# Optimization experiments

Hardware: AMD Instinct MI355X
Metric: run time of the kernel (lower is better)

Reference implementation:

```python
import jax, jax.numpy as jnp
import numpy as np

B, N, E = 4096, 32, 64
IN_DIM, H = 74, 256
ADD_DIM = 2
MLP1, MLP2 = 1024, 512
GCR_LAYERS = 5


def setup_inputs() -> dict:
    key = jax.random.key(0)
    ks = jax.random.split(key, 26)
    s = 0.05
    inp = {
        "x": jax.random.normal(ks[0], (B, N, IN_DIM), jnp.float32),
        "add_features": jax.random.normal(ks[1], (B, ADD_DIM), jnp.float32),
        "src": jax.random.randint(ks[2], (B, E), 0, N, jnp.int32),
        "dst": jax.random.randint(ks[3], (B, E), 0, N, jnp.int32),
        # first GraphConv (in_dim -> hidden)
        "W_in": jax.random.normal(ks[4], (IN_DIM, H), jnp.float32) * s,
        "b_in": jnp.zeros((H,), jnp.float32),
        # 5 GCR blocks, each with two GraphConv layers (hidden -> hidden)
        "W_g1": jax.random.normal(ks[5], (GCR_LAYERS, H, H), jnp.float32) * s,
        "b_g1": jnp.zeros((GCR_LAYERS, H), jnp.float32),
        "W_g2": jax.random.normal(ks[6], (GCR_LAYERS, H, H), jnp.float32) * s,
        "b_g2": jnp.zeros((GCR_LAYERS, H), jnp.float32),
        # attention pooling
        "Wq": jax.random.normal(ks[7], (H, H), jnp.float32) * s,
        "bq": jnp.zeros((H,), jnp.float32),
        "Wk": jax.random.normal(ks[8], (H, H), jnp.float32) * s,
        "bk": jnp.zeros((H,), jnp.float32),
        "Wv": jax.random.normal(ks[9], (H, 1), jnp.float32) * s,
        "bv": jnp.zeros((1,), jnp.float32),
        "W_m1": jax.random.normal(ks[10], (H + ADD_DIM, MLP1), jnp.float32) * s,
        "b_m1": jnp.zeros((MLP1,), jnp.float32),
        "W_m2": jax.random.normal(ks[11], (MLP1, MLP2), jnp.float32) * s,
        "b_m2": jnp.zeros((MLP2,), jnp.float32),
        "W_m3": jax.random.normal(ks[12], (MLP2, 1), jnp.float32) * s,
        "b_m3": jnp.zeros((1,), jnp.float32),
    }
    return inp


def _forward(x, add_features, src, dst, W_in, b_in, W_g1, b_g1, W_g2, b_g2,
             Wq, bq, Wk, bk, Wv, bv, W_m1, b_m1, W_m2, b_m2, W_m3, b_m3):
    def per_graph(xg, sg, dg):
        # DGL GraphConv norm='both': D_out^{-1/2} on src side, D_in^{-1/2} on dst side
        ones = jnp.ones((E,), xg.dtype)
        out_deg = jnp.zeros((N,), xg.dtype).at[sg].add(ones)
        in_deg = jnp.zeros((N,), xg.dtype).at[dg].add(ones)
        onorm = jax.lax.rsqrt(jnp.clip(out_deg, 1.0))
        inorm = jax.lax.rsqrt(jnp.clip(in_deg, 1.0))

        def conv(h, W, b):
            h = (h * onorm[:, None]) @ W                      # [N, out]
            agg = jnp.zeros((N, W.shape[1]), h.dtype).at[dg].add(h[sg])
            return agg * inorm[:, None] + b

        h = conv(xg, W_in, b_in)
        for i in range(GCR_LAYERS):
            t = conv(h, W_g1[i], b_g1[i])
            t = conv(jax.nn.relu(t), W_g2[i], b_g2[i])
            h = jax.nn.relu(t)                                # GCR output (res_connection=0)
        # attention-weighted pooling over nodes
        q = h @ Wq + bq                                       # [N, H]
        k = h @ Wk + bk                                       # [N, H]
        v = h @ Wv + bv                                       # [N, 1]
        attn = jax.nn.softmax(q @ k.T, axis=1)                # [N, N]
        w = (attn @ v)[:, 0]                                  # [N]
        return h.T @ w                                        # [H]

    feats = jax.vmap(per_graph)(x, src, dst)                  # [B, H]
    z = jnp.concatenate([feats, add_features], axis=1)        # [B, H+ADD_DIM]
    z = jax.nn.leaky_relu(z @ W_m1 + b_m1)
    z = jax.nn.leaky_relu(z @ W_m2 + b_m2)
    z = z @ W_m3 + b_m3                                       # [B, 1]
    return z[:, 0]


def reference(x, add_features, src, dst, W_in, b_in, W_g1, b_g1, W_g2, b_g2,
              Wq, bq, Wk, bk, Wv, bv, W_m1, b_m1, W_m2, b_m2, W_m3, b_m3):
    return _forward(x, add_features, src, dst, W_in, b_in, W_g1, b_g1, W_g2, b_g2,
                    Wq, bq, Wk, bk, Wv, bv, W_m1, b_m1, W_m2, b_m2, W_m3, b_m3)
```

## Files before the change

kernel.cpp:

```cpp
#include <hip/hip_runtime.h>
#include <math.h>

#define BB     4096
#define NN     32
#define EE     64
#define INDIM  74
#define HH     256
#define GCR    5
#define M1     1024
#define M2     512
#define FDIM   258
#define ADDD   2
#define FSTR   288

typedef __attribute__((ext_vector_type(8))) _Float16 half8_t;
typedef __attribute__((ext_vector_type(4))) float float4_t;

#define MF16(a, b, c) __builtin_amdgcn_mfma_f32_16x16x32_f16((a), (b), (c), 0, 0, 0)
#define LO_SCALE 1024.0f
#define LO_INV   (1.0f / 1024.0f)

#define WS_FH     0
#define WS_WQK    4227072
#define WS_TVEC   4489216
#define WS_PK     4490240
#define PK_WIN_HI 0
#define PK_WIN_LO 24576
#define PK_G_BASE 49152
#define PK_G_STRIDE 131072
#define PK_WQK_HI 1359872
#define PK_WQK_LO (1359872 + 65536)
#define PK_W1P    1490944
#define PK_W2P    1785856

union H4 { unsigned long long u; _Float16 h[4]; };

__global__ void prep1_kernel(const float* __restrict__ Wq, const float* __restrict__ Wk,
                             const float* __restrict__ bq,
                             float* __restrict__ wqkf, float* __restrict__ tvec) {
  const int i = blockIdx.x, j = threadIdx.x;
  if (i < 256) {
    __shared__ float qrow[256];
    qrow[j] = Wq[i * 256 + j];
    __syncthreads();
    float s = 0.f;
    for (int c = 0; c < 256; ++c) s = fmaf(qrow[c], Wk[j * 256 + c], s);
    wqkf[i * 256 + j] = s;
  } else {
    float s = 0.f;
    for (int c = 0; c < 256; ++c) s = fmaf(Wk[j * 256 + c], bq[c], s);
    tvec[j] = s;
  }
}

template<int KS, int KREAL>
__device__ __forceinline__ void pack_one(const float* __restrict__ S,
                                         _Float16* __restrict__ hi,
                                         _Float16* __restrict__ lo, int local) {
  const int l = local & 63;
  const int nk = local >> 6;
  const int ks = nk % KS;
  const int nt = nk / KS;
  const int j = nt * 16 + (l & 15);
  const int kbase = ks * 32 + (l >> 4) * 8;
  half8_t h8, l8;
  #pragma unroll
  for (int i = 0; i < 8; ++i) {
    const int k = kbase + i;
    const float v = (k < KREAL) ? S[k * 256 + j] : 0.f;
    const _Float16 hb = (_Float16)v;
    h8[i] = hb;
    l8[i] = (_Float16)((v - (float)hb) * LO_SCALE);
  }
  *(half8_t*)(hi + (size_t)local * 8) = h8;
  *(half8_t*)(lo + (size_t)local * 8) = l8;
}

__global__ void prep2_kernel(const float* __restrict__ W_in,
                             const float* __restrict__ W_g1, const float* __restrict__ W_g2,
                             const float* __restrict__ wqkf, _Float16* __restrict__ pk) {
  const int cid = blockIdx.x * 256 + threadIdx.x;
  if (cid < 3072) {
    pack_one<3, 74>(W_in, pk + PK_WIN_HI, pk + PK_WIN_LO, cid);
  } else {
    const int m = (cid - 3072) >> 13;
    const int local = (cid - 3072) & 8191;
    _Float16* hi; const float* S;
    if (m < 10) {
      hi = pk + PK_G_BASE + (size_t)m * PK_G_STRIDE;
      S = (m < 5) ? (W_g1 + (size_t)m * 65536) : (W_g2 + (size_t)(m - 5) * 65536);
    } else {
      hi = pk + PK_WQK_HI;
      S = wqkf;
    }
    pack_one<8, 256>(S, hi, hi + 65536, local);
  }
}

template<int KS, int KREAL, int NCOL>
__device__ __forceinline__ void pack_flat(const float* __restrict__ S,
                                          _Float16* __restrict__ dst, int local) {
  const int l = local & 63;
  const int nk = local >> 6;
  const int ks = nk % KS;
  const int nt = nk / KS;
  const int j = nt * 16 + (l & 15);
  const int kbase = ks * 32 + (l >> 4) * 8;
  half8_t h8;
  #pragma unroll
  for (int i = 0; i < 8; ++i) {
    const int k = kbase + i;
    h8[i] = (_Float16)((k < KREAL) ? S[(size_t)k * NCOL + j] : 0.f);
  }
  *(half8_t*)(dst + (size_t)local * 8) = h8;
}

__global__ void prep3_kernel(const float* __restrict__ W1, const float* __restrict__ W2,
                             _Float16* __restrict__ pk) {
  const int cid = blockIdx.x * 256 + threadIdx.x;
  if (cid < 36864) {
    pack_flat<9, 258, 1024>(W1, pk + PK_W1P, cid);
  } else {
    pack_flat<32, 1024, 512>(W2, pk + PK_W2P, cid - 36864);
  }
}

template<int KS, bool RELU>
__device__ __forceinline__ void conv2x(
    _Float16* Hs, _Float16* Tb, const _Float16* NmF,
    const _Float16* __restrict__ Whi,
    const float* __restrict__ bias,
    int lane, int wv)
{
  const int g4 = lane >> 4, l15 = lane & 15;
  const int sw = l15 << 3;

  #pragma unroll
  for (int p = 0; p < 2; ++p) {
    const int nt = p * 8 + wv;
    float4_t th[2][2];
    #pragma unroll
    for (int a = 0; a < 2; ++a)
      #pragma unroll
      for (int b = 0; b < 2; ++b)
        th[a][b] = (float4_t){0.f, 0.f, 0.f, 0.f};
    #pragma unroll
    for (int ks = 0; ks < KS; ++ks) {
      const int off = ((nt * KS + ks) * 64 + lane) * 8;
      const half8_t wh = *(const half8_t*)(Whi + off);
      const int j0 = ks * 32 + g4 * 8;
      #pragma unroll
      for (int gi = 0; gi < 2; ++gi)
        #pragma unroll
        for (int mt = 0; mt < 2; ++mt) {
          const half8_t ha = *(const half8_t*)(Hs + (gi << 13) + ((mt * 16 + l15) * 256 + (j0 ^ sw)));
          th[gi][mt] = MF16(ha, wh, th[gi][mt]);
        }
    }
    #pragma unroll
    for (int gi = 0; gi < 2; ++gi)
      #pragma unroll
      for (int mt = 0; mt < 2; ++mt) {
        const int r0 = mt * 16 + 4 * g4;
        H4 pk4;
        #pragma unroll
        for (int jj = 0; jj < 4; ++jj)
          pk4.h[jj] = (_Float16)th[gi][mt][jj];
        const int idx = nt * 512 + ((r0 >> 3) * 16 + l15) * 8 + (r0 & 7);
        *(unsigned long long*)(Tb + (gi << 13) + idx) = pk4.u;
      }
  }

  __syncthreads();

  #pragma unroll
  for (int p = 0; p < 2; ++p) {
    const int nt = p * 8 + wv;
    const float4 b4 = *(const float4*)&bias[nt * 16 + 4 * g4];
    const int j0 = nt * 16 + 4 * g4;
    #pragma unroll
    for (int gi = 0; gi < 2; ++gi) {
      const half8_t ta = *(const half8_t*)(Tb + (gi << 13) + nt * 512 + lane * 8);
      #pragma unroll
      for (int nt2 = 0; nt2 < 2; ++nt2) {
        const half8_t nmh = *(const half8_t*)(NmF + ((gi * 2 + nt2) * 64 + lane) * 8);
        const float4_t dh = MF16(ta, nmh, ((float4_t){0.f, 0.f, 0.f, 0.f}));
        H4 pk4;
        #pragma unroll
        for (int jj = 0; jj < 4; ++jj) {
          float v = dh[jj] + ((const float*)&b4)[jj];
          if (RELU) v = fmaxf(v, 0.f);
          pk4.h[jj] = (_Float16)v;
        }
        const int n = nt2 * 16 + l15;
        *(unsigned long long*)(Hs + (gi << 13) + (n * 256 + (j0 ^ ((n & 15) << 3)))) = pk4.u;
      }
    }
  }
  __syncthreads();
}

__global__ __launch_bounds__(512, 4)
void gnn_kernel(const float* __restrict__ x, const float* __restrict__ addf,
                const int* __restrict__ src, const int* __restrict__ dst,
                const float* __restrict__ b_in,
                const float* __restrict__ b_g1, const float* __restrict__ b_g2,
                const float* __restrict__ Wvp, const float* __restrict__ bv,
                const _Float16* __restrict__ pk,
                const float* __restrict__ tvec,
                _Float16* __restrict__ Fh)
{
  __shared__ __align__(16) _Float16 Hs[2][8192];
  __shared__ __align__(16) _Float16 Tb[2][8192];
  __shared__ __align__(16) _Float16 NmF[2048];
  __shared__ float Sb[2][1184];

  const int tid = threadIdx.x;
  const int lane = tid & 63;
  const int wv = tid >> 6;
  const int g4 = lane >> 4, l15 = lane & 15;
  const int sw = l15 << 3;
  const int ga = blockIdx.x * 2;

  for (int i = tid; i < 2048; i += 512) Sb[i >> 10][i & 1023] = 0.f;
  __syncthreads();
  if (tid < 128) {
    const int gi = tid >> 6, e = tid & 63;
    const int es = src[(size_t)(ga + gi) * EE + e];
    const int ed = dst[(size_t)(ga + gi) * EE + e];
    atomicAdd(&Sb[gi][ed * 32 + es], 1.0f);
  }
  __syncthreads();
  if (tid < 64) {
    const int gi = tid >> 5, n = tid & 31;
    float s = 0.f;
    for (int m = 0; m < NN; ++m) s += Sb[gi][n * 32 + m];
    Sb[gi][1056 + n] = 1.f / sqrtf(fmaxf(s, 1.f));
  } else if (tid < 128) {
    const int gi = (tid - 64) >> 5, n = tid & 31;
    float s = 0.f;
    for (int m = 0; m < NN; ++m) s += Sb[gi][m * 32 + n];
    Sb[gi][1088 + n] = 1.f / sqrtf(fmaxf(s, 1.f));
  }
  __syncthreads();
  for (int i = tid; i < 2048; i += 512) {
    const int gi = i >> 10, idx = i & 1023;
    Sb[gi][idx] *= Sb[gi][1056 + (idx >> 5)] * Sb[gi][1088 + (idx & 31)];
  }
  __syncthreads();

  if (wv == 0) {
    #pragma unroll
    for (int gi = 0; gi < 2; ++gi) {
      #pragma unroll
      for (int nt2 = 0; nt2 < 2; ++nt2) {
        half8_t h8;
        #pragma unroll
        for (int i = 0; i < 8; ++i)
          h8[i] = (_Float16)Sb[gi][(nt2 * 16 + l15) * 32 + g4 * 8 + i];
        *(half8_t*)(NmF + ((gi * 2 + nt2) * 64 + lane) * 8) = h8;
      }
    }
  }

  for (int i = tid; i < 2 * NN * 96; i += 512) {
    const int gi = i / 3072, rem = i - gi * 3072;
    const int r = rem / 96, c = rem - r * 96;
    const float vx = (c < INDIM) ? x[(size_t)(ga + gi) * (NN * INDIM) + r * INDIM + c] : 0.f;
    Hs[gi][r * 256 + (c ^ ((r & 15) << 3))] = (_Float16)vx;
  }
  __syncthreads();

  conv2x<3, false>(&Hs[0][0], &Tb[0][0], NmF, pk + PK_WIN_HI, b_in, lane, wv);
  #pragma unroll 1
  for (int L = 0; L < GCR; ++L) {
    conv2x<8, true>(&Hs[0][0], &Tb[0][0], NmF,
                    pk + PK_G_BASE + (size_t)L * PK_G_STRIDE, b_g1 + L * HH, lane, wv);
    conv2x<8, true>(&Hs[0][0], &Tb[0][0], NmF,
                    pk + PK_G_BASE + (size_t)(5 + L) * PK_G_STRIDE, b_g2 + L * HH, lane, wv);
  }

  {
    const _Float16* Qhi = pk + PK_WQK_HI;
    const int sgi = wv >> 2, smt = (wv >> 1) & 1, snt = wv & 1;
    float4_t sacc = (float4_t){0.f, 0.f, 0.f, 0.f};

    #pragma unroll
    for (int p = 0; p < 2; ++p) {
      const int nt = p * 8 + wv;
      float4_t uh[2][2];
      #pragma unroll
      for (int a = 0; a < 2; ++a)
        #pragma unroll
        for (int b = 0; b < 2; ++b)
          uh[a][b] = (float4_t){0.f, 0.f, 0.f, 0.f};
      #pragma unroll
      for (int ks = 0; ks < 8; ++ks) {
        const int off = ((nt * 8 + ks) * 64 + lane) * 8;
        const half8_t qh = *(const half8_t*)(Qhi + off);
        const int j0 = ks * 32 + g4 * 8;
        #pragma unroll
        for (int gi = 0; gi < 2; ++gi)
          #pragma unroll
          for (int mt = 0; mt < 2; ++mt) {
            const half8_t ha = *(const half8_t*)(&Hs[gi][(mt * 16 + l15) * 256 + (j0 ^ sw)]);
            uh[gi][mt] = MF16(ha, qh, uh[gi][mt]);
          }
      }
      const float tv = tvec[nt * 16 + l15];
      const int cl = wv * 16 + l15;
      #pragma unroll
      for (int gi = 0; gi < 2; ++gi)
        #pragma unroll
        for (int mt = 0; mt < 2; ++mt)
          #pragma unroll
          for (int jj = 0; jj < 4; ++jj) {
            const int n = mt * 16 + 4 * g4 + jj;
            Tb[gi][n * 128 + (cl ^ ((n & 15) << 3))] =
                (_Float16)(uh[gi][mt][jj] + tv);
          }
      __syncthreads();
      #pragma unroll
      for (int ksl = 0; ksl < 4; ++ksl) {
        const int kl = ksl * 32 + g4 * 8;
        const half8_t ua = *(const half8_t*)(&Tb[sgi][(smt * 16 + l15) * 128 + (kl ^ sw)]);
        const half8_t hb = *(const half8_t*)(&Hs[sgi][(snt * 16 + l15) * 256 + ((p * 128 + kl) ^ sw)]);
        sacc = MF16(ua, hb, sacc);
      }
      __syncthreads();
    }
    #pragma unroll
    for (int jj = 0; jj < 4; ++jj)
      Sb[sgi][(smt * 16 + 4 * g4 + jj) * 33 + snt * 16 + l15] = sacc[jj];
  }

  {
    const int gi = tid >> 8, m = (tid >> 3) & 31, q = tid & 7;
    float s = 0.f;
    const int c0 = q * 32;
    for (int cc = 0; cc < 32; ++cc) {
      const int c = c0 + cc;
      s = fmaf((float)Hs[gi][m * 256 + (c ^ ((m & 15) << 3))], Wvp[c], s);
    }
    s += __shfl_xor(s, 1);
    s += __shfl_xor(s, 2);
    s += __shfl_xor(s, 4);
    if (q == 0) Sb[gi][1120 + m] = s + bv[0];
  }
  __syncthreads();

  if (tid < 64) {
    const int gi = tid >> 5, n = tid & 31;
    float mx = -1e30f;
    #pragma unroll 1
    for (int m = 0; m < NN; ++m) mx = fmaxf(mx, Sb[gi][n * 33 + m]);
    float se = 0.f, sv = 0.f;
    #pragma unroll 1
    for (int m = 0; m < NN; ++m) {
      const float e = expf(Sb[gi][n * 33 + m] - mx);
      se += e;
      sv = fmaf(e, Sb[gi][1120 + m], sv);
    }
    Sb[gi][1152 + n] = sv / se;
  }
  __syncthreads();

  {
    const int gi = tid >> 8, j = tid & 255;
    float f0 = 0.f;
    #pragma unroll
    for (int m = 0; m < NN; ++m) {
      const float w = Sb[gi][1152 + m];
      f0 = fmaf((float)Hs[gi][m * 256 + (j ^ ((m & 15) << 3))], w, f0);
    }
    Fh[(size_t)(ga + gi) * FSTR + j] = (_Float16)f0;
    if (tid < 64) {
      const int g2 = tid >> 5, c = 256 + (tid & 31);
      Fh[(size_t)(ga + g2) * FSTR + c] =
          (c < FDIM) ? (_Float16)addf[(size_t)(ga + g2) * ADDD + (c - 256)] : (_Float16)0.f;
    }
  }
}

__global__ __launch_bounds__(512, 4)
void mlp_kernel(const _Float16* __restrict__ Fh,
                const _Float16* __restrict__ W1p, const float* __restrict__ b1,
                const _Float16* __restrict__ W2p, const float* __restrict__ b2,
                const float* __restrict__ W3, const float* __restrict__ b3,
                float* __restrict__ out)
{
  __shared__ __align__(16) _Float16 Ft[16 * 320];
  __shared__ __align__(16) _Float16 Z1[16 * 1024];
  __shared__ __align__(16) _Float16 Z2[16 * 512];

  const int tid = threadIdx.x, lane = tid & 63, wv = tid >> 6;
  const int g4 = lane >> 4, l15 = lane & 15;
  const int sw = (l15 & 7) << 3;
  const int r0 = blockIdx.x * 16;

  for (int i = tid; i < 16 * FSTR; i += 512) {
    const int r = i / FSTR, c = i - r * FSTR;
    Ft[r * 320 + (c ^ ((r & 7) << 3))] = Fh[(size_t)(r0 + r) * FSTR + c];
  }
  __syncthreads();

  {
    float4_t a1[8];
    #pragma unroll
    for (int t = 0; t < 8; ++t) a1[t] = (float4_t){0.f, 0.f, 0.f, 0.f};
    #pragma unroll
    for (int ks = 0; ks < 9; ++ks) {
      const half8_t fb = *(const half8_t*)(Ft + l15 * 320 + ((ks * 32 + g4 * 8) ^ sw));
      #pragma unroll
      for (int t = 0; t < 8; ++t) {
        const int jt = wv * 8 + t;
        const half8_t wf = *(const half8_t*)(W1p + ((size_t)(jt * 9 + ks) * 64 + lane) * 8);
        a1[t] = MF16(wf, fb, a1[t]);
      }
    }
    #pragma unroll
    for (int t = 0; t < 8; ++t) {
      const int j0 = (wv * 8 + t) * 16 + 4 * g4;
      const float4 bb = *(const float4*)&b1[j0];
      H4 pk4;
      #pragma unroll
      for (int jj = 0; jj < 4; ++jj) {
        const float z = a1[t][jj] + ((const float*)&bb)[jj];
        pk4.h[jj] = (_Float16)fmaxf(z, 0.01f * z);
      }
      *(unsigned long long*)(Z1 + l15 * 1024 + (j0 ^ sw)) = pk4.u;
    }
  }
  __syncthreads();

  {
    float4_t a2[4];
    #pragma unroll
    for (int t = 0; t < 4; ++t) a2[t] = (float4_t){0.f, 0.f, 0.f, 0.f};
    #pragma unroll 4
    for (int ks = 0; ks < 32; ++ks) {
      const half8_t zb = *(const half8_t*)(Z1 + l15 * 1024 + ((ks * 32 + g4 * 8) ^ sw));
      #pragma unroll
      for (int t = 0; t < 4; ++t) {
        const int jt = wv * 4 + t;
        const half8_t wf = *(const half8_t*)(W2p + ((size_t)(jt * 32 + ks) * 64 + lane) * 8);
        a2[t] = MF16(wf, zb, a2[t]);
      }
    }
    #pragma unroll
    for (int t = 0; t < 4; ++t) {
      const int j0 = (wv * 4 + t) * 16 + 4 * g4;
      const float4 bb = *(const float4*)&b2[j0];
      H4 pk4;
      #pragma unroll
      for (int jj = 0; jj < 4; ++jj) {
        const float z = a2[t][jj] + ((const float*)&bb)[jj];
        pk4.h[jj] = (_Float16)fmaxf(z, 0.01f * z);
      }
      *(unsigned long long*)(Z2 + l15 * 512 + (j0 ^ sw)) = pk4.u;
    }
  }
  __syncthreads();

  {
    const int m = tid >> 5, q = tid & 31;
    const int swm = (m & 7) << 3;
    float s = 0.f;
    #pragma unroll
    for (int h = 0; h < 2; ++h) {
      const int c0 = q * 16 + h * 8;
      const half8_t z8 = *(const half8_t*)(Z2 + m * 512 + (c0 ^ swm));
      #pragma unroll
      for (int i2 = 0; i2 < 8; ++i2)
        s = fmaf((float)z8[i2], W3[c0 + i2], s);
    }
    s += __shfl_xor(s, 1);
    s += __shfl_xor(s, 2);
    s += __shfl_xor(s, 4);
    s += __shfl_xor(s, 8);
    s += __shfl_xor(s, 16);
    if (q == 0) out[r0 + m] = s + b3[0];
  }
}

extern "C" void kernel_launch(void* const* d_in, const int* in_sizes, int n_in,
                              void* d_out, int out_size, void* d_ws, size_t ws_size,
                              hipStream_t stream) {
  (void)in_sizes; (void)n_in; (void)out_size; (void)ws_size;
  const float* x    = (const float*)d_in[0];
  const float* addf = (const float*)d_in[1];
  const int*   src  = (const int*)d_in[2];
  const int*   dst  = (const int*)d_in[3];
  const float* W_in = (const float*)d_in[4];
  const float* b_in = (const float*)d_in[5];
  const float* W_g1 = (const float*)d_in[6];
  const float* b_g1 = (const float*)d_in[7];
  const float* W_g2 = (const float*)d_in[8];
  const float* b_g2 = (const float*)d_in[9];
  const float* Wq   = (const float*)d_in[10];
  const float* bq   = (const float*)d_in[11];
  const float* Wk   = (const float*)d_in[12];
  const float* Wv   = (const float*)d_in[14];
  const float* bv   = (const float*)d_in[15];
  const float* W1   = (const float*)d_in[16];
  const float* b1   = (const float*)d_in[17];
  const float* W2   = (const float*)d_in[18];
  const float* b2   = (const float*)d_in[19];
  const float* W3   = (const float*)d_in[20];
  const float* b3   = (const float*)d_in[21];
  float* out = (float*)d_out;

  _Float16* Fh    = (_Float16*)((char*)d_ws + WS_FH);
  float* wqkf     = (float*)((char*)d_ws + WS_WQK);
  float* tvec     = (float*)((char*)d_ws + WS_TVEC);
  _Float16* pk    = (_Float16*)((char*)d_ws + WS_PK);

  prep1_kernel<<<dim3(257), dim3(256), 0, stream>>>(Wq, Wk, bq, wqkf, tvec);
  prep2_kernel<<<dim3(364), dim3(256), 0, stream>>>(W_in, W_g1, W_g2, wqkf, pk);
  prep3_kernel<<<dim3(400), dim3(256), 0, stream>>>(W1, W2, pk);
  gnn_kernel<<<dim3(BB / 2), dim3(512), 0, stream>>>(
      x, addf, src, dst, b_in, b_g1, b_g2, Wv, bv, pk, tvec, Fh);
  mlp_kernel<<<dim3(BB / 16), dim3(512), 0, stream>>>(
      Fh, pk + PK_W1P, b1, pk + PK_W2P, b2, W3, b3, out);
}
```

Measured before the change: 279.9 us.

## Reuse H fragments across both column tiles and keep norm matrix in registers

Each GraphConv's dense GEMM now computes both N-tiles per wave in a single K loop, so every H fragment read from LDS feeds two MFMAs instead of being reloaded per tile pass. The normalized adjacency fragments are held in registers per wave rather than staged through a shared buffer. The Q·K attention score stage writes the full 256-wide projected tile first and then runs one 8-step reduction, which removes a pair of barriers. The trade-off is twice as many live accumulators, which raises register pressure at 512 threads with launch bounds of 4 blocks.

Result: slower. 341.4 us (+22.0%).

```diff
diff --git a/kernel.cpp b/kernel.cpp
--- a/kernel.cpp
+++ b/kernel.cpp
@@ -18,7 +18,6 @@
 
 #define MF16(a, b, c) __builtin_amdgcn_mfma_f32_16x16x32_f16((a), (b), (c), 0, 0, 0)
 #define LO_SCALE 1024.0f
-#define LO_INV   (1.0f / 1024.0f)
 
 #define WS_FH     0
 #define WS_WQK    4227072
@@ -127,7 +126,8 @@
 
 template<int KS, bool RELU>
 __device__ __forceinline__ void conv2x(
-    _Float16* Hs, _Float16* Tb, const _Float16* NmF,
+    _Float16* Hs, _Float16* Tb,
+    const half8_t nm[2][2],
     const _Float16* __restrict__ Whi,
     const float* __restrict__ bias,
     int lane, int wv)
@@ -135,28 +135,33 @@
   const int g4 = lane >> 4, l15 = lane & 15;
   const int sw = l15 << 3;
 
-  #pragma unroll
-  for (int p = 0; p < 2; ++p) {
-    const int nt = p * 8 + wv;
-    float4_t th[2][2];
-    #pragma unroll
-    for (int a = 0; a < 2; ++a)
-      #pragma unroll
-      for (int b = 0; b < 2; ++b)
-        th[a][b] = (float4_t){0.f, 0.f, 0.f, 0.f};
-    #pragma unroll
-    for (int ks = 0; ks < KS; ++ks) {
-      const int off = ((nt * KS + ks) * 64 + lane) * 8;
-      const half8_t wh = *(const half8_t*)(Whi + off);
-      const int j0 = ks * 32 + g4 * 8;
-      #pragma unroll
-      for (int gi = 0; gi < 2; ++gi)
-        #pragma unroll
-        for (int mt = 0; mt < 2; ++mt) {
-          const half8_t ha = *(const half8_t*)(Hs + (gi << 13) + ((mt * 16 + l15) * 256 + (j0 ^ sw)));
-          th[gi][mt] = MF16(ha, wh, th[gi][mt]);
-        }
-    }
+  float4_t th[2][2][2];
+  #pragma unroll
+  for (int a = 0; a < 2; ++a)
+    #pragma unroll
+    for (int b = 0; b < 2; ++b)
+      #pragma unroll
+      for (int c = 0; c < 2; ++c)
+        th[a][b][c] = (float4_t){0.f, 0.f, 0.f, 0.f};
+
+  #pragma unroll
+  for (int ks = 0; ks < KS; ++ks) {
+    const half8_t wh0 = *(const half8_t*)(Whi + ((wv * KS + ks) * 64 + lane) * 8);
+    const half8_t wh1 = *(const half8_t*)(Whi + (((8 + wv) * KS + ks) * 64 + lane) * 8);
+    const int j0 = ks * 32 + g4 * 8;
+    #pragma unroll
+    for (int gi = 0; gi < 2; ++gi)
+      #pragma unroll
+      for (int mt = 0; mt < 2; ++mt) {
+        const half8_t ha = *(const half8_t*)(Hs + (gi << 13) + ((mt * 16 + l15) * 256 + (j0 ^ sw)));
+        th[0][gi][mt] = MF16(ha, wh0, th[0][gi][mt]);
+        th[1][gi][mt] = MF16(ha, wh1, th[1][gi][mt]);
+      }
+  }
+
+  #pragma unroll
+  for (int ni = 0; ni < 2; ++ni) {
+    const int nt = ni * 8 + wv;
     #pragma unroll
     for (int gi = 0; gi < 2; ++gi)
       #pragma unroll
@@ -165,7 +170,7 @@
         H4 pk4;
         #pragma unroll
         for (int jj = 0; jj < 4; ++jj)
-          pk4.h[jj] = (_Float16)th[gi][mt][jj];
+          pk4.h[jj] = (_Float16)th[ni][gi][mt][jj];
         const int idx = nt * 512 + ((r0 >> 3) * 16 + l15) * 8 + (r0 & 7);
         *(unsigned long long*)(Tb + (gi << 13) + idx) = pk4.u;
       }
@@ -174,8 +179,8 @@
   __syncthreads();
 
   #pragma unroll
-  for (int p = 0; p < 2; ++p) {
-    const int nt = p * 8 + wv;
+  for (int ni = 0; ni < 2; ++ni) {
+    const int nt = ni * 8 + wv;
     const float4 b4 = *(const float4*)&bias[nt * 16 + 4 * g4];
     const int j0 = nt * 16 + 4 * g4;
     #pragma unroll
@@ -183,8 +188,7 @@
       const half8_t ta = *(const half8_t*)(Tb + (gi << 13) + nt * 512 + lane * 8);
       #pragma unroll
       for (int nt2 = 0; nt2 < 2; ++nt2) {
-        const half8_t nmh = *(const half8_t*)(NmF + ((gi * 2 + nt2) * 64 + lane) * 8);
-        const float4_t dh = MF16(ta, nmh, ((float4_t){0.f, 0.f, 0.f, 0.f}));
+        const float4_t dh = MF16(ta, nm[gi][nt2], ((float4_t){0.f, 0.f, 0.f, 0.f}));
         H4 pk4;
         #pragma unroll
         for (int jj = 0; jj < 4; ++jj) {
@@ -212,7 +216,6 @@
 {
   __shared__ __align__(16) _Float16 Hs[2][8192];
   __shared__ __align__(16) _Float16 Tb[2][8192];
-  __shared__ __align__(16) _Float16 NmF[2048];
   __shared__ float Sb[2][1184];
 
   const int tid = threadIdx.x;
@@ -249,19 +252,14 @@
   }
   __syncthreads();
 
-  if (wv == 0) {
-    #pragma unroll
-    for (int gi = 0; gi < 2; ++gi) {
-      #pragma unroll
-      for (int nt2 = 0; nt2 < 2; ++nt2) {
-        half8_t h8;
-        #pragma unroll
-        for (int i = 0; i < 8; ++i)
-          h8[i] = (_Float16)Sb[gi][(nt2 * 16 + l15) * 32 + g4 * 8 + i];
-        *(half8_t*)(NmF + ((gi * 2 + nt2) * 64 + lane) * 8) = h8;
-      }
-    }
-  }
+  half8_t nm[2][2];
+  #pragma unroll
+  for (int gi = 0; gi < 2; ++gi)
+    #pragma unroll
+    for (int nt2 = 0; nt2 < 2; ++nt2)
+      #pragma unroll
+      for (int i = 0; i < 8; ++i)
+        nm[gi][nt2][i] = (_Float16)Sb[gi][(nt2 * 16 + l15) * 32 + g4 * 8 + i];
 
   for (int i = tid; i < 2 * NN * 96; i += 512) {
     const int gi = i / 3072, rem = i - gi * 3072;
@@ -271,44 +269,47 @@
   }
   __syncthreads();
 
-  conv2x<3, false>(&Hs[0][0], &Tb[0][0], NmF, pk + PK_WIN_HI, b_in, lane, wv);
+  conv2x<3, false>(&Hs[0][0], &Tb[0][0], nm, pk + PK_WIN_HI, b_in, lane, wv);
   #pragma unroll 1
   for (int L = 0; L < GCR; ++L) {
-    conv2x<8, true>(&Hs[0][0], &Tb[0][0], NmF,
+    conv2x<8, true>(&Hs[0][0], &Tb[0][0], nm,
                     pk + PK_G_BASE + (size_t)L * PK_G_STRIDE, b_g1 + L * HH, lane, wv);
-    conv2x<8, true>(&Hs[0][0], &Tb[0][0], NmF,
+    conv2x<8, true>(&Hs[0][0], &Tb[0][0], nm,
                     pk + PK_G_BASE + (size_t)(5 + L) * PK_G_STRIDE, b_g2 + L * HH, lane, wv);
   }
 
   {
     const _Float16* Qhi = pk + PK_WQK_HI;
     const int sgi = wv >> 2, smt = (wv >> 1) & 1, snt = wv & 1;
-    float4_t sacc = (float4_t){0.f, 0.f, 0.f, 0.f};
-
-    #pragma unroll
-    for (int p = 0; p < 2; ++p) {
-      const int nt = p * 8 + wv;
-      float4_t uh[2][2];
-      #pragma unroll
-      for (int a = 0; a < 2; ++a)
+
+    float4_t uh[2][2][2];
+    #pragma unroll
+    for (int a = 0; a < 2; ++a)
+      #pragma unroll
+      for (int b = 0; b < 2; ++b)
         #pragma unroll
-        for (int b = 0; b < 2; ++b)
-          uh[a][b] = (float4_t){0.f, 0.f, 0.f, 0.f};
-      #pragma unroll
-      for (int ks = 0; ks < 8; ++ks) {
-        const int off = ((nt * 8 + ks) * 64 + lane) * 8;
-        const half8_t qh = *(const half8_t*)(Qhi + off);
-        const int j0 = ks * 32 + g4 * 8;
+        for (int c = 0; c < 2; ++c)
+          uh[a][b][c] = (float4_t){0.f, 0.f, 0.f, 0.f};
+
+    #pragma unroll
+    for (int ks = 0; ks < 8; ++ks) {
+      const half8_t qh0 = *(const half8_t*)(Qhi + ((wv * 8 + ks) * 64 + lane) * 8);
+      const half8_t qh1 = *(const half8_t*)(Qhi + (((8 + wv) * 8 + ks) * 64 + lane) * 8);
+      const int j0 = ks * 32 + g4 * 8;
+      #pragma unroll
+      for (int gi = 0; gi < 2; ++gi)
         #pragma unroll
-        for (int gi = 0; gi < 2; ++gi)
-          #pragma unroll
-          for (int mt = 0; mt < 2; ++mt) {
-            const half8_t ha = *(const half8_t*)(&Hs[gi][(mt * 16 + l15) * 256 + (j0 ^ sw)]);
-            uh[gi][mt] = MF16(ha, qh, uh[gi][mt]);
-          }
-      }
+        for (int mt = 0; mt < 2; ++mt) {
+          const half8_t ha = *(const half8_t*)(&Hs[gi][(mt * 16 + l15) * 256 + (j0 ^ sw)]);
+          uh[0][gi][mt] = MF16(ha, qh0, uh[0][gi][mt]);
+          uh[1][gi][mt] = MF16(ha, qh1, uh[1][gi][mt]);
+        }
+    }
+    #pragma unroll
+    for (int ni = 0; ni < 2; ++ni) {
+      const int nt = ni * 8 + wv;
       const float tv = tvec[nt * 16 + l15];
-      const int cl = wv * 16 + l15;
+      const int cl = nt * 16 + l15;
       #pragma unroll
       for (int gi = 0; gi < 2; ++gi)
         #pragma unroll
@@ -316,18 +317,18 @@
           #pragma unroll
           for (int jj = 0; jj < 4; ++jj) {
             const int n = mt * 16 + 4 * g4 + jj;
-            Tb[gi][n * 128 + (cl ^ ((n & 15) << 3))] =
-                (_Float16)(uh[gi][mt][jj] + tv);
+            Tb[gi][n * 256 + (cl ^ ((n & 15) << 3))] =
+                (_Float16)(uh[ni][gi][mt][jj] + tv);
           }
-      __syncthreads();
-      #pragma unroll
-      for (int ksl = 0; ksl < 4; ++ksl) {
-        const int kl = ksl * 32 + g4 * 8;
-        const half8_t ua = *(const half8_t*)(&Tb[sgi][(smt * 16 + l15) * 128 + (kl ^ sw)]);
-        const half8_t hb = *(const half8_t*)(&Hs[sgi][(snt * 16 + l15) * 256 + ((p * 128 + kl) ^ sw)]);
-        sacc = MF16(ua, hb, sacc);
-      }
-      __syncthreads();
+    }
+    __syncthreads();
+    float4_t sacc = (float4_t){0.f, 0.f, 0.f, 0.f};
+    #pragma unroll
+    for (int ksl = 0; ksl < 8; ++ksl) {
+      const int kl = ksl * 32 + g4 * 8;
+      const half8_t ua = *(const half8_t*)(&Tb[sgi][(smt * 16 + l15) * 256 + (kl ^ sw)]);
+      const half8_t hb = *(const half8_t*)(&Hs[sgi][(snt * 16 + l15) * 256 + (kl ^ sw)]);
+      sacc = MF16(ua, hb, sacc);
     }
     #pragma unroll
     for (int jj = 0; jj < 4; ++jj)
```
